# Optimization experiments

Hardware: AMD Instinct MI355X
Metric: run time of the kernel (lower is better)

## Reference

```python
import jax, jax.numpy as jnp
import numpy as np

LPC_ORDER = 32
GAMMA = 1.0  # get_gamma(1, None) == 1


def setup_inputs() -> dict:
    key = jax.random.key(0)
    # PARCOR coefficients, magnitude < 1 for stability; shape (..., M+1)
    k = jax.random.uniform(key, (16, 65536, LPC_ORDER + 1), dtype=jnp.float32)
    return {"k": k}


def reference(k):
    # Levinson-style PARCOR -> LPC recursion (diffsptk par2lpc).
    # a starts as k / gamma; for m = 2..M: a[1:m] += k[m] * flip(a[1:m])
    M1 = k.shape[-1]
    a = k / GAMMA
    for m in range(2, M1):  # fixed, small unrolled loop over order
        km = k[..., m : m + 1]          # (..., 1)  reflection coefficient
        am = a[..., 1:m]                 # (..., m-1) current LPC prefix
        a = a.at[..., 1:m].set(am + km * am[..., ::-1])
    return a
```

## Files before the change

kernel.cpp:

```cpp
#include <hip/hip_runtime.h>

#define M1   33
#define BLK  128
#define BLK_ELEMS (BLK * M1)
#define BLK_VEC4  (BLK_ELEMS / 4)
#define VEC_FULL  (BLK_VEC4 / BLK)
#define VEC_REM   (BLK_VEC4 - VEC_FULL * BLK)

__global__ __launch_bounds__(BLK)
void parcor_to_lpc_kernel(const float* __restrict__ k, float* __restrict__ out) {
    __shared__ float lds[BLK_ELEMS];

    const size_t base = (size_t)blockIdx.x * BLK_ELEMS;
    const float4* __restrict__ gsrc4 = (const float4*)(k + base);
    float4* __restrict__ gdst4 = (float4*)(out + base);
    float4* lds4 = (float4*)lds;

    #pragma unroll
    for (int i = 0; i < VEC_FULL; ++i)
        lds4[i * BLK + threadIdx.x] = gsrc4[i * BLK + threadIdx.x];
    if (threadIdx.x < VEC_REM)
        lds4[VEC_FULL * BLK + threadIdx.x] = gsrc4[VEC_FULL * BLK + threadIdx.x];
    __syncthreads();

    const int t = threadIdx.x;
    float a[M1];
    #pragma unroll
    for (int j = 0; j < M1; ++j)
        a[j] = lds[t * M1 + j];

    #pragma unroll
    for (int m = 2; m < M1; ++m) {
        const float km = a[m];
        #pragma unroll
        for (int j = 1; 2 * j < m; ++j) {
            const float x = a[j];
            const float y = a[m - j];
            a[j]     = fmaf(km, y, x);
            a[m - j] = fmaf(km, x, y);
        }
        if ((m & 1) == 0) {
            const int j = m >> 1;
            a[j] = fmaf(km, a[j], a[j]);
        }
    }

    #pragma unroll
    for (int j = 0; j < M1; ++j)
        lds[t * M1 + j] = a[j];
    __syncthreads();

    #pragma unroll
    for (int i = 0; i < VEC_FULL; ++i)
        gdst4[i * BLK + threadIdx.x] = lds4[i * BLK + threadIdx.x];
    if (threadIdx.x < VEC_REM)
        gdst4[VEC_FULL * BLK + threadIdx.x] = lds4[VEC_FULL * BLK + threadIdx.x];
}

__global__ void parcor_to_lpc_tail_kernel(const float* __restrict__ k,
                                          float* __restrict__ out,
                                          int row_start, int nrows) {
    const int row = row_start + blockIdx.x * blockDim.x + threadIdx.x;
    if (row >= nrows) return;
    const float* src = k + (size_t)row * M1;
    float* dst = out + (size_t)row * M1;
    float a[M1];
    #pragma unroll
    for (int j = 0; j < M1; ++j) a[j] = src[j];
    #pragma unroll
    for (int m = 2; m < M1; ++m) {
        const float km = a[m];
        #pragma unroll
        for (int j = 1; 2 * j < m; ++j) {
            const float x = a[j];
            const float y = a[m - j];
            a[j]     = fmaf(km, y, x);
            a[m - j] = fmaf(km, x, y);
        }
        if ((m & 1) == 0) {
            const int j = m >> 1;
            a[j] = fmaf(km, a[j], a[j]);
        }
    }
    #pragma unroll
    for (int j = 0; j < M1; ++j) dst[j] = a[j];
}

extern "C" void kernel_launch(void* const* d_in, const int* in_sizes, int n_in,
                              void* d_out, int out_size, void* d_ws, size_t ws_size,
                              hipStream_t stream) {
    const float* k = (const float*)d_in[0];
    float* out = (float*)d_out;

    const int nrows = in_sizes[0] / M1;
    const int nblk  = nrows / BLK;
    const int rem   = nrows - nblk * BLK;

    if (nblk > 0)
        parcor_to_lpc_kernel<<<nblk, BLK, 0, stream>>>(k, out);
    if (rem > 0)
        parcor_to_lpc_tail_kernel<<<(rem + BLK - 1) / BLK, BLK, 0, stream>>>(
            k, out, nblk * BLK, nrows);
}
```

Before: 238.5 us.

## Process four rows per thread with direct float4 global loads, dropping LDS staging

Each thread now handles four consecutive rows (132 floats, 33 float4s), loading and storing them straight from global memory with float4 accesses instead of staging a block's rows through shared memory. This removes the LDS round trip and both barriers, and gives each thread four independent recursions to interleave for ILP. In exchange, per-thread register use grows sharply (about 132 live floats), so occupancy drops. Global accesses are now strided across lanes (each lane touches its own 528-byte span), which may hurt coalescing.

```diff
diff --git a/kernel.cpp b/kernel.cpp
--- a/kernel.cpp
+++ b/kernel.cpp
@@ -1,60 +1,49 @@
 #include <hip/hip_runtime.h>
 
 #define M1   33
-#define BLK  128
-#define BLK_ELEMS (BLK * M1)
-#define BLK_VEC4  (BLK_ELEMS / 4)
-#define VEC_FULL  (BLK_VEC4 / BLK)
-#define VEC_REM   (BLK_VEC4 - VEC_FULL * BLK)
+#define RPT  4
+#define BLK  64
+#define FPT  (RPT * M1)
+#define VPT  (FPT / 4)
 
-__global__ __launch_bounds__(BLK)
-void parcor_to_lpc_kernel(const float* __restrict__ k, float* __restrict__ out) {
-    __shared__ float lds[BLK_ELEMS];
+__global__ __launch_bounds__(BLK, 3)
+void parcor_to_lpc_kernel(const float* __restrict__ k, float* __restrict__ out,
+                          int nthreads) {
+    const int tid = blockIdx.x * BLK + threadIdx.x;
+    if (tid >= nthreads) return;
 
-    const size_t base = (size_t)blockIdx.x * BLK_ELEMS;
-    const float4* __restrict__ gsrc4 = (const float4*)(k + base);
-    float4* __restrict__ gdst4 = (float4*)(out + base);
-    float4* lds4 = (float4*)lds;
+    const float4* __restrict__ src = (const float4*)k   + (size_t)tid * VPT;
+    float4*       __restrict__ dst = (float4*)out       + (size_t)tid * VPT;
+
+    union { float f[FPT]; float4 v[VPT]; } a;
 
     #pragma unroll
-    for (int i = 0; i < VEC_FULL; ++i)
-        lds4[i * BLK + threadIdx.x] = gsrc4[i * BLK + threadIdx.x];
-    if (threadIdx.x < VEC_REM)
-        lds4[VEC_FULL * BLK + threadIdx.x] = gsrc4[VEC_FULL * BLK + threadIdx.x];
-    __syncthreads();
-
-    const int t = threadIdx.x;
-    float a[M1];
-    #pragma unroll
-    for (int j = 0; j < M1; ++j)
-        a[j] = lds[t * M1 + j];
+    for (int i = 0; i < VPT; ++i)
+        a.v[i] = src[i];
 
     #pragma unroll
     for (int m = 2; m < M1; ++m) {
-        const float km = a[m];
         #pragma unroll
-        for (int j = 1; 2 * j < m; ++j) {
-            const float x = a[j];
-            const float y = a[m - j];
-            a[j]     = fmaf(km, y, x);
-            a[m - j] = fmaf(km, x, y);
-        }
-        if ((m & 1) == 0) {
-            const int j = m >> 1;
-            a[j] = fmaf(km, a[j], a[j]);
+        for (int r = 0; r < RPT; ++r) {
+            float* ar = a.f + r * M1;
+            const float km = ar[m];
+            #pragma unroll
+            for (int j = 1; 2 * j < m; ++j) {
+                const float x = ar[j];
+                const float y = ar[m - j];
+                ar[j]     = fmaf(km, y, x);
+                ar[m - j] = fmaf(km, x, y);
+            }
+            if ((m & 1) == 0) {
+                const int j = m >> 1;
+                ar[j] = fmaf(km, ar[j], ar[j]);
+            }
         }
     }
 
     #pragma unroll
-    for (int j = 0; j < M1; ++j)
-        lds[t * M1 + j] = a[j];
-    __syncthreads();
-
-    #pragma unroll
-    for (int i = 0; i < VEC_FULL; ++i)
-        gdst4[i * BLK + threadIdx.x] = lds4[i * BLK + threadIdx.x];
-    if (threadIdx.x < VEC_REM)
-        gdst4[VEC_FULL * BLK + threadIdx.x] = lds4[VEC_FULL * BLK + threadIdx.x];
+    for (int i = 0; i < VPT; ++i)
+        dst[i] = a.v[i];
 }
 
 __global__ void parcor_to_lpc_tail_kernel(const float* __restrict__ k,
@@ -92,13 +81,16 @@
     const float* k = (const float*)d_in[0];
     float* out = (float*)d_out;
 
-    const int nrows = in_sizes[0] / M1;
-    const int nblk  = nrows / BLK;
-    const int rem   = nrows - nblk * BLK;
+    const int nrows    = in_sizes[0] / M1;
+    const int nthreads = nrows / RPT;
+    const int rem_row0 = nthreads * RPT;
+    const int rem      = nrows - rem_row0;
 
-    if (nblk > 0)
-        parcor_to_lpc_kernel<<<nblk, BLK, 0, stream>>>(k, out);
+    if (nthreads > 0) {
+        const int nblk = (nthreads + BLK - 1) / BLK;
+        parcor_to_lpc_kernel<<<nblk, BLK, 0, stream>>>(k, out, nthreads);
+    }
     if (rem > 0)
-        parcor_to_lpc_tail_kernel<<<(rem + BLK - 1) / BLK, BLK, 0, stream>>>(
-            k, out, nblk * BLK, nrows);
+        parcor_to_lpc_tail_kernel<<<(rem + 63) / 64, 64, 0, stream>>>(
+            k, out, rem_row0, nrows);
 }
```

New measurement: 377.8 us. 1.58x slower.

## Persistent single-wave blocks with double-buffered async global-to-LDS tile prefetch

Applied to the files above, without the earlier changes.

Switches to a persistent grid of single-wavefront (64-thread) blocks that loop over 64-row tiles. Each iteration prefetches the next tile straight into a second LDS buffer with global_load_lds DMA, and manual s_waitcnt replaces __syncthreads. The goal is to overlap global loads with the recursion and stores, and to drop block barriers and the register round-trip on loads. The risks are lower per-CU occupancy, which can limit latency hiding on a memory-bound kernel, and fragile hand-written vmcnt counts. There is also no barrier between the async LDS writes and the other lanes' reads, which relies on single-wave execution.

```diff
diff --git a/kernel.cpp b/kernel.cpp
--- a/kernel.cpp
+++ b/kernel.cpp
@@ -1,60 +1,90 @@
 #include <hip/hip_runtime.h>
 
-#define M1   33
-#define BLK  128
-#define BLK_ELEMS (BLK * M1)
-#define BLK_VEC4  (BLK_ELEMS / 4)
-#define VEC_FULL  (BLK_VEC4 / BLK)
-#define VEC_REM   (BLK_VEC4 - VEC_FULL * BLK)
+#define M1      33
+#define TROWS   64
+#define BLK     64
+#define TILE_F  (TROWS * M1)
+#define NLD     8
+#define NST     8
+#define PARTIAL 16
+#define GRID    2304
+
+typedef const __attribute__((address_space(1))) float* gptr_t;
+typedef __attribute__((address_space(3))) float*       lptr_t;
+
+__device__ __forceinline__ void stage_tile(const float* __restrict__ g,
+                                           float* lds_base, int lane) {
+    #pragma unroll
+    for (int i = 0; i < NLD; ++i)
+        __builtin_amdgcn_global_load_lds((gptr_t)(g + i * 256 + lane * 4),
+                                         (lptr_t)(lds_base + i * 256), 16, 0, 0);
+    if (lane < PARTIAL)
+        __builtin_amdgcn_global_load_lds((gptr_t)(g + NLD * 256 + lane * 4),
+                                         (lptr_t)(lds_base + NLD * 256), 16, 0, 0);
+}
 
 __global__ __launch_bounds__(BLK)
-void parcor_to_lpc_kernel(const float* __restrict__ k, float* __restrict__ out) {
-    __shared__ float lds[BLK_ELEMS];
+void parcor_to_lpc_kernel(const float* __restrict__ k, float* __restrict__ out,
+                          int ntiles) {
+    __shared__ __align__(16) float lds[2 * TILE_F];
+    const int lane = threadIdx.x;
 
-    const size_t base = (size_t)blockIdx.x * BLK_ELEMS;
-    const float4* __restrict__ gsrc4 = (const float4*)(k + base);
-    float4* __restrict__ gdst4 = (float4*)(out + base);
-    float4* lds4 = (float4*)lds;
+    int tile = blockIdx.x;
+    if (tile >= ntiles) return;
+    const int stride = gridDim.x;
 
-    #pragma unroll
-    for (int i = 0; i < VEC_FULL; ++i)
-        lds4[i * BLK + threadIdx.x] = gsrc4[i * BLK + threadIdx.x];
-    if (threadIdx.x < VEC_REM)
-        lds4[VEC_FULL * BLK + threadIdx.x] = gsrc4[VEC_FULL * BLK + threadIdx.x];
-    __syncthreads();
+    stage_tile(k + (size_t)tile * TILE_F, &lds[0], lane);
 
-    const int t = threadIdx.x;
-    float a[M1];
-    #pragma unroll
-    for (int j = 0; j < M1; ++j)
-        a[j] = lds[t * M1 + j];
+    int buf = 0;
+    bool first = true;
+    while (true) {
+        const int next = tile + stride;
 
-    #pragma unroll
-    for (int m = 2; m < M1; ++m) {
-        const float km = a[m];
+        if (first) { asm volatile("s_waitcnt vmcnt(0)" ::: "memory"); first = false; }
+        else       { asm volatile("s_waitcnt vmcnt(9)" ::: "memory"); }
+
+        if (next < ntiles)
+            stage_tile(k + (size_t)next * TILE_F, &lds[(buf ^ 1) * TILE_F], lane);
+
+        float* L = &lds[buf * TILE_F];
+
+        float a[M1];
         #pragma unroll
-        for (int j = 1; 2 * j < m; ++j) {
-            const float x = a[j];
-            const float y = a[m - j];
-            a[j]     = fmaf(km, y, x);
-            a[m - j] = fmaf(km, x, y);
+        for (int j = 0; j < M1; ++j) a[j] = L[lane * M1 + j];
+
+        #pragma unroll
+        for (int m = 2; m < M1; ++m) {
+            const float km = a[m];
+            #pragma unroll
+            for (int j = 1; 2 * j < m; ++j) {
+                const float x = a[j];
+                const float y = a[m - j];
+                a[j]     = fmaf(km, y, x);
+                a[m - j] = fmaf(km, x, y);
+            }
+            if ((m & 1) == 0) {
+                const int j = m >> 1;
+                a[j] = fmaf(km, a[j], a[j]);
+            }
         }
-        if ((m & 1) == 0) {
-            const int j = m >> 1;
-            a[j] = fmaf(km, a[j], a[j]);
-        }
+
+        #pragma unroll
+        for (int j = 0; j < M1; ++j) L[lane * M1 + j] = a[j];
+
+        asm volatile("s_waitcnt lgkmcnt(0)" ::: "memory");
+
+        const float4* l4 = (const float4*)L;
+        float4* g4 = (float4*)(out + (size_t)tile * TILE_F);
+        #pragma unroll
+        for (int i = 0; i < NST; ++i)
+            g4[i * BLK + lane] = l4[i * BLK + lane];
+        if (lane < PARTIAL)
+            g4[NST * BLK + lane] = l4[NST * BLK + lane];
+
+        if (next >= ntiles) break;
+        tile = next;
+        buf ^= 1;
     }
-
-    #pragma unroll
-    for (int j = 0; j < M1; ++j)
-        lds[t * M1 + j] = a[j];
-    __syncthreads();
-
-    #pragma unroll
-    for (int i = 0; i < VEC_FULL; ++i)
-        gdst4[i * BLK + threadIdx.x] = lds4[i * BLK + threadIdx.x];
-    if (threadIdx.x < VEC_REM)
-        gdst4[VEC_FULL * BLK + threadIdx.x] = lds4[VEC_FULL * BLK + threadIdx.x];
 }
 
 __global__ void parcor_to_lpc_tail_kernel(const float* __restrict__ k,
@@ -92,13 +122,16 @@
     const float* k = (const float*)d_in[0];
     float* out = (float*)d_out;
 
-    const int nrows = in_sizes[0] / M1;
-    const int nblk  = nrows / BLK;
-    const int rem   = nrows - nblk * BLK;
+    const int nrows     = in_sizes[0] / M1;
+    const int ntiles    = nrows / TROWS;
+    const int tile_rows = ntiles * TROWS;
+    const int rem       = nrows - tile_rows;
 
-    if (nblk > 0)
-        parcor_to_lpc_kernel<<<nblk, BLK, 0, stream>>>(k, out);
+    if (ntiles > 0) {
+        const int grid = ntiles < GRID ? ntiles : GRID;
+        parcor_to_lpc_kernel<<<grid, BLK, 0, stream>>>(k, out, ntiles);
+    }
     if (rem > 0)
-        parcor_to_lpc_tail_kernel<<<(rem + BLK - 1) / BLK, BLK, 0, stream>>>(
-            k, out, nblk * BLK, nrows);
+        parcor_to_lpc_tail_kernel<<<(rem + 63) / 64, 64, 0, stream>>>(
+            k, out, tile_rows, nrows);
 }
```

Measured after the change: 239.8 us. Within noise of the previous version (+0.6%).
